# Kernel optimization log

Measured on AMD Instinct MI355X. Metric: run time of the kernel, lower is better.

The kernel has to match this reference:

```python
import jax, jax.numpy as jnp
import numpy as np

EPS = 1e-12  # F.normalize eps

def _l2_normalize(x):
    n = jnp.linalg.norm(x, axis=-1, keepdims=True)
    return x / jnp.maximum(n, EPS)

def setup_inputs() -> dict:
    key = jax.random.key(0)
    k1, k2 = jax.random.split(key)
    B, C, F = 32768, 1000, 256
    features = jax.random.normal(k1, (B, F), dtype=jnp.float32)
    prototypes = jax.random.normal(k2, (C, F), dtype=jnp.float32)
    distance_scale = jnp.ones((1,), dtype=jnp.float32)
    temperature = jnp.ones((1,), dtype=jnp.float32)
    return {"features": features, "prototypes": prototypes,
            "distance_scale": distance_scale, "temperature": temperature}

def reference(features, prototypes, distance_scale, temperature):
    # Normalize both sides to the unit sphere (F.normalize, p=2, eps=1e-12)
    fn = _l2_normalize(features)       # [B, F]
    pn = _l2_normalize(prototypes)     # [C, F]
    # For unit vectors: ||a-b||_2 / sqrt(2) = sqrt(1 - a.b)
    cos = jnp.einsum('bf,cf->bc', fn, pn)          # [B, C]
    dist = jnp.sqrt(jnp.maximum(1.0 - cos, 0.0))   # cdist(...)/sqrt(2)
    iso = jnp.abs(distance_scale[0]) * dist
    logits = -(iso + jnp.mean(iso, axis=1, keepdims=True))
    return logits / temperature[0]
```

## Files before the change

### kernel.cpp

```cpp
#include <hip/hip_runtime.h>


typedef __attribute__((ext_vector_type(8))) short short8;
typedef __attribute__((ext_vector_type(4))) float f32x4;
typedef __fp16 h2 __attribute__((ext_vector_type(2)));

union U16 { uint4 u4; short8 s8; };

static __device__ __forceinline__ unsigned short f2bf(float x){
  union { float f; unsigned u; } v; v.f = x;
  unsigned r = v.u + 0x7fffu + ((v.u >> 16) & 1u);
  return (unsigned short)(r >> 16);
}

#define CPAD 1024

__global__ void norm_protos_kernel(const float* __restrict__ src,
                                   unsigned short* __restrict__ dst, int C)
{
  const int wave = threadIdx.x >> 6;
  const int lane = threadIdx.x & 63;
  const int row  = blockIdx.x * 4 + wave;
  const int t    = row >> 4;
  const int l16  = row & 15;
  const int s    = lane >> 3;
  const int quad = (lane >> 1) & 3;
  const int j    = (lane & 1) * 4;

  ushort4 o = {0, 0, 0, 0};
  if (row < C){
    const float4 v = *(const float4*)(src + row * 256 + lane * 4);
    float ss = v.x*v.x + v.y*v.y + v.z*v.z + v.w*v.w;
    #pragma unroll
    for (int off = 32; off; off >>= 1) ss += __shfl_xor(ss, off);
    const float inv = 1.0f / fmaxf(sqrtf(ss), 1e-12f);
    o.x = f2bf(v.x * inv); o.y = f2bf(v.y * inv);
    o.z = f2bf(v.z * inv); o.w = f2bf(v.w * inv);
  }
  *(ushort4*)(dst + ((size_t)((t*8 + s)*64 + quad*16 + l16))*8 + j) = o;
}

__global__ __launch_bounds__(256, 2)
void fused_kernel(const float* __restrict__ feats,
                  const unsigned short* __restrict__ pnw,
                  const float* __restrict__ ds,
                  const float* __restrict__ temp,
                  float* __restrict__ out, int C)
{
  __shared__ float wsum[2][16][4];

  const int tid  = threadIdx.x;
  const int wave = tid >> 6;
  const int lane = tid & 63;
  const int quad = lane >> 4;
  const int l16  = lane & 15;
  const long rowbase = (long)blockIdx.x * 32;

  short8 ffrag[2][8];
  #pragma unroll
  for (int rg = 0; rg < 2; ++rg){
    const float* rp = feats + (rowbase + rg*16 + l16) * 256 + quad*8;
    float4 va[8], vb[8];
    float ss = 0.f;
    #pragma unroll
    for (int s = 0; s < 8; ++s){
      va[s] = *(const float4*)(rp + s*32);
      vb[s] = *(const float4*)(rp + s*32 + 4);
      ss += va[s].x*va[s].x + va[s].y*va[s].y + va[s].z*va[s].z + va[s].w*va[s].w;
      ss += vb[s].x*vb[s].x + vb[s].y*vb[s].y + vb[s].z*vb[s].z + vb[s].w*vb[s].w;
    }
    ss += __shfl_xor(ss, 16);
    ss += __shfl_xor(ss, 32);
    const float inv = __builtin_amdgcn_rcpf(__builtin_amdgcn_sqrtf(fmaxf(ss, 1e-24f)));
    #pragma unroll
    for (int s = 0; s < 8; ++s){
      U16 u;
      u.u4.x = (unsigned)f2bf(va[s].x*inv) | ((unsigned)f2bf(va[s].y*inv) << 16);
      u.u4.y = (unsigned)f2bf(va[s].z*inv) | ((unsigned)f2bf(va[s].w*inv) << 16);
      u.u4.z = (unsigned)f2bf(vb[s].x*inv) | ((unsigned)f2bf(vb[s].y*inv) << 16);
      u.u4.w = (unsigned)f2bf(vb[s].z*inv) | ((unsigned)f2bf(vb[s].w*inv) << 16);
      ffrag[rg][s] = u.s8;
    }
  }

  const uint4* tp = (const uint4*)pnw + (size_t)(wave*16)*512 + lane;

  h2 dd0[16][2];
  h2 dd1[16][2];
  float rsum0 = 0.f, rsum1 = 0.f;

  #pragma unroll
  for (int wt = 0; wt < 16; ++wt){
    const uint4* bp = tp + (size_t)wt*512;
    short8 pfrag[8];
    #pragma unroll
    for (int s = 0; s < 8; ++s){ U16 u; u.u4 = bp[s*64]; pfrag[s] = u.s8; }

    f32x4 acc0 = (f32x4){0.f, 0.f, 0.f, 0.f};
    f32x4 acc1 = (f32x4){0.f, 0.f, 0.f, 0.f};
    #pragma unroll
    for (int s = 0; s < 8; ++s){
      acc0 = __builtin_amdgcn_mfma_f32_16x16x32_bf16(pfrag[s], ffrag[0][s], acc0, 0, 0, 0);
      acc1 = __builtin_amdgcn_mfma_f32_16x16x32_bf16(pfrag[s], ffrag[1][s], acc1, 0, 0, 0);
    }

    float a0 = __builtin_amdgcn_sqrtf(fmaxf(1.0f - acc0[0], 0.0f));
    float a1 = __builtin_amdgcn_sqrtf(fmaxf(1.0f - acc0[1], 0.0f));
    float a2 = __builtin_amdgcn_sqrtf(fmaxf(1.0f - acc0[2], 0.0f));
    float a3 = __builtin_amdgcn_sqrtf(fmaxf(1.0f - acc0[3], 0.0f));
    float b0 = __builtin_amdgcn_sqrtf(fmaxf(1.0f - acc1[0], 0.0f));
    float b1 = __builtin_amdgcn_sqrtf(fmaxf(1.0f - acc1[1], 0.0f));
    float b2 = __builtin_amdgcn_sqrtf(fmaxf(1.0f - acc1[2], 0.0f));
    float b3 = __builtin_amdgcn_sqrtf(fmaxf(1.0f - acc1[3], 0.0f));

    const int cls = wave*256 + wt*16 + quad*4;
    rsum0 += (cls < C) ? (a0 + a1 + a2 + a3) : 0.0f;
    rsum1 += (cls < C) ? (b0 + b1 + b2 + b3) : 0.0f;

    dd0[wt][0] = __builtin_amdgcn_cvt_pkrtz(a0, a1);
    dd0[wt][1] = __builtin_amdgcn_cvt_pkrtz(a2, a3);
    dd1[wt][0] = __builtin_amdgcn_cvt_pkrtz(b0, b1);
    dd1[wt][1] = __builtin_amdgcn_cvt_pkrtz(b2, b3);
  }

  rsum0 += __shfl_xor(rsum0, 16);
  rsum0 += __shfl_xor(rsum0, 32);
  rsum1 += __shfl_xor(rsum1, 16);
  rsum1 += __shfl_xor(rsum1, 32);
  if (quad == 0){
    wsum[0][l16][wave] = rsum0;
    wsum[1][l16][wave] = rsum1;
  }
  __syncthreads();

  const float nscale = -fabsf(ds[0]) / temp[0];
  const float4 w0 = *(const float4*)&wsum[0][l16][0];
  const float4 w1 = *(const float4*)&wsum[1][l16][0];
  const float bias0 = nscale * ((w0.x + w0.y + w0.z + w0.w) / (float)C);
  const float bias1 = nscale * ((w1.x + w1.y + w1.z + w1.w) / (float)C);

  float* orow0 = out + (rowbase + l16) * (size_t)C;
  float* orow1 = out + (rowbase + 16 + l16) * (size_t)C;
  #pragma unroll
  for (int wt = 0; wt < 16; ++wt){
    const int cls = wave*256 + wt*16 + quad*4;
    if (cls < C){
      float4 o0, o1;
      o0.x = fmaf(nscale, (float)dd0[wt][0][0], bias0);
      o0.y = fmaf(nscale, (float)dd0[wt][0][1], bias0);
      o0.z = fmaf(nscale, (float)dd0[wt][1][0], bias0);
      o0.w = fmaf(nscale, (float)dd0[wt][1][1], bias0);
      o1.x = fmaf(nscale, (float)dd1[wt][0][0], bias1);
      o1.y = fmaf(nscale, (float)dd1[wt][0][1], bias1);
      o1.z = fmaf(nscale, (float)dd1[wt][1][0], bias1);
      o1.w = fmaf(nscale, (float)dd1[wt][1][1], bias1);
      *(float4*)(orow0 + cls) = o0;
      *(float4*)(orow1 + cls) = o1;
    }
  }
}

extern "C" void kernel_launch(void* const* d_in, const int* in_sizes, int n_in,
                              void* d_out, int out_size, void* d_ws, size_t ws_size,
                              hipStream_t stream) {
  const float* features = (const float*)d_in[0];
  const float* protos   = (const float*)d_in[1];
  const float* dscale   = (const float*)d_in[2];
  const float* temp     = (const float*)d_in[3];
  float* out = (float*)d_out;

  const int F = 256;
  const int B = in_sizes[0] / F;
  const int C = in_sizes[1] / F;

  unsigned short* pnw = (unsigned short*)d_ws;

  norm_protos_kernel<<<CPAD/4, 256, 0, stream>>>(protos, pnw, C);
  fused_kernel<<<B/32, 256, 0, stream>>>(features, pnw, dscale, temp, out, C);
}
```

Baseline: 189.3 us.

## Double-buffer prototype tiles in LDS via async global_load_lds prefetch

Prototype fragments were previously loaded straight from global memory into registers on each tile iteration. Now each wave streams them into its own two-slot LDS ring using async global-to-LDS loads, issued two tiles ahead, with explicit vmcnt waits and scheduling barriers. It also raises wave priority around the MFMA block. The aim is to hide global/L2 latency of the prototype loads behind MFMA and epilogue work. The cost is 64KB of LDS per block, which could affect occupancy, plus hand-placed waits and barriers that limit the compiler's scheduling freedom.

Measured after the change: 186.4 us. No clear change (-1.6%).

```diff
diff --git a/kernel.cpp b/kernel.cpp
--- a/kernel.cpp
+++ b/kernel.cpp
@@ -40,6 +40,11 @@
   *(ushort4*)(dst + ((size_t)((t*8 + s)*64 + quad*16 + l16))*8 + j) = o;
 }
 
+#define VMWAIT8 do{ asm volatile("s_waitcnt vmcnt(8)" ::: "memory"); \
+                    __builtin_amdgcn_sched_barrier(0); }while(0)
+#define VMWAIT0 do{ asm volatile("s_waitcnt vmcnt(0)" ::: "memory"); \
+                    __builtin_amdgcn_sched_barrier(0); }while(0)
+
 __global__ __launch_bounds__(256, 2)
 void fused_kernel(const float* __restrict__ feats,
                   const unsigned short* __restrict__ pnw,
@@ -47,6 +52,7 @@
                   const float* __restrict__ temp,
                   float* __restrict__ out, int C)
 {
+  __shared__ uint4 pring[4][2][512];
   __shared__ float wsum[2][16][4];
 
   const int tid  = threadIdx.x;
@@ -83,7 +89,21 @@
     }
   }
 
-  const uint4* tp = (const uint4*)pnw + (size_t)(wave*16)*512 + lane;
+  const uint4* tpg = (const uint4*)pnw + (size_t)(wave*16)*512 + lane;
+
+  #define STAGE(wt, slot) do{                                               \
+      const uint4* g_ = tpg + (size_t)(wt)*512;                             \
+      _Pragma("unroll")                                                     \
+      for (int s_ = 0; s_ < 8; ++s_)                                        \
+        __builtin_amdgcn_global_load_lds(                                   \
+          (const __attribute__((address_space(1))) void*)(g_ + s_*64),      \
+          (__attribute__((address_space(3))) void*)(&pring[wave][slot][s_*64]), \
+          16, 0, 0);                                                        \
+    }while(0)
+
+  __builtin_amdgcn_sched_barrier(0);
+  STAGE(0, 0);
+  STAGE(1, 1);
 
   h2 dd0[16][2];
   h2 dd1[16][2];
@@ -91,17 +111,26 @@
 
   #pragma unroll
   for (int wt = 0; wt < 16; ++wt){
-    const uint4* bp = tp + (size_t)wt*512;
+    if (wt < 15) { VMWAIT8; } else { VMWAIT0; }
+
+    const uint4* l = &pring[wave][wt & 1][0];
     short8 pfrag[8];
     #pragma unroll
-    for (int s = 0; s < 8; ++s){ U16 u; u.u4 = bp[s*64]; pfrag[s] = u.s8; }
+    for (int s = 0; s < 8; ++s){ U16 u; u.u4 = l[s*64 + lane]; pfrag[s] = u.s8; }
 
     f32x4 acc0 = (f32x4){0.f, 0.f, 0.f, 0.f};
     f32x4 acc1 = (f32x4){0.f, 0.f, 0.f, 0.f};
+    __builtin_amdgcn_s_setprio(1);
     #pragma unroll
     for (int s = 0; s < 8; ++s){
       acc0 = __builtin_amdgcn_mfma_f32_16x16x32_bf16(pfrag[s], ffrag[0][s], acc0, 0, 0, 0);
       acc1 = __builtin_amdgcn_mfma_f32_16x16x32_bf16(pfrag[s], ffrag[1][s], acc1, 0, 0, 0);
+    }
+    __builtin_amdgcn_s_setprio(0);
+
+    if (wt + 2 < 16){
+      __builtin_amdgcn_sched_barrier(0);
+      STAGE(wt + 2, wt & 1);
     }
 
     float a0 = __builtin_amdgcn_sqrtf(fmaxf(1.0f - acc0[0], 0.0f));
@@ -122,6 +151,7 @@
     dd1[wt][0] = __builtin_amdgcn_cvt_pkrtz(b0, b1);
     dd1[wt][1] = __builtin_amdgcn_cvt_pkrtz(b2, b3);
   }
+  #undef STAGE
 
   rsum0 += __shfl_xor(rsum0, 16);
   rsum0 += __shfl_xor(rsum0, 32);
```
